# Kernel tuning notes

Hardware: AMD Instinct MI355X
Metric: run time of the kernel (lower is better)

## Reference

```python
import jax, jax.numpy as jnp
import numpy as np

S, B, T, D, NUM_CH = 16, 64, 640, 256, 4
T_WAV = 1.0 / 16000.0
LOG_F_MEAN = 5.02654
LOG_F_STD = 0.373288


def _make_i_2pi(output_dim, num_channels):
    num_freq = output_dim // num_channels
    # harmonic index i+1 repeated num_channels times, times 2*pi -> (D, 1)
    i_vec = np.repeat(np.arange(1, num_freq + 1, dtype=np.float32), num_channels)
    return jnp.asarray(i_vec * (2.0 * np.pi)).reshape(output_dim, 1)


def _make_k_T(time_len):
    # sample times 0..T-1 scaled by 1/16000 -> (1, T)
    return (jnp.arange(time_len, dtype=jnp.float32) * T_WAV).reshape(1, time_len)


def setup_inputs() -> dict:
    key = jax.random.key(0)
    k1, k2, k3, k4, k5 = jax.random.split(key, 5)
    x = jax.random.normal(k1, (S, B, 1, T), dtype=jnp.float32)
    nlf = jax.random.normal(k2, (S, B, 1, 1), dtype=jnp.float32)
    tau = jax.random.uniform(k3, (S, B, 1, 1), dtype=jnp.float32) * (T * T_WAV)
    a = jax.random.normal(k4, (D, 1), dtype=jnp.float32)
    phi = jax.random.normal(k5, (D, 1), dtype=jnp.float32)
    return {"x": x, "nlf": nlf, "tau": tau, "a": a, "phi": phi,
            "i_2pi": _make_i_2pi(D, NUM_CH), "k_T": _make_k_T(T)}


def reference(x, nlf, tau, a, phi, i_2pi, k_T):
    # f: denormalized fundamental frequency, (S,B,1,1)
    f = jnp.exp(nlf * LOG_F_STD + LOG_F_MEAN)
    # t: shifted time axis, (S,B,1,T)
    t = k_T - tau
    # deg = i*2pi*f*t + phi -> (S,B,D,T)
    i_f = i_2pi * f            # (S,B,D,1)
    deg = i_f * t + phi        # (S,B,D,T)
    W = a * jnp.sin(deg)       # (S,B,D,T)
    h_SBDT = W * x             # (S,B,D,T)  <- the huge intermediate
    return jnp.sum(h_SBDT, axis=-1)  # (S,B,D)
```

## Files before the change

kernel.cpp:

```cpp
#include <hip/hip_runtime.h>

constexpr int S_  = 16;
constexpr int B_  = 64;
constexpr int T_  = 640;
constexpr int D_  = 256;
constexpr int H_  = 64;
constexpr int SB_ = S_ * B_;

__device__ __forceinline__ float fractf_(float x) { return __builtin_amdgcn_fractf(x); }
__device__ __forceinline__ float sin2pi_(float r) { return __builtin_amdgcn_sinf(r); }

struct GQ { double g, q; };

__global__ void sinenet_pre(const float* __restrict__ nlf,
                            const float* __restrict__ tau,
                            const float* __restrict__ a,
                            const float* __restrict__ phi,
                            GQ* __restrict__ gq,
                            float* __restrict__ ca,
                            float* __restrict__ sa)
{
    const int idx = blockIdx.x * 256 + threadIdx.x;
    if (idx < SB_) {
        const double fd = exp((double)nlf[idx] * 0.373288 + 5.02654);
        GQ v;
        v.g = fd * (1.0 / 16000.0);
        v.q = fd * (double)tau[idx];
        gq[idx] = v;
    } else if (idx < SB_ + D_) {
        const int d  = idx - SB_;
        const float av = a[d];
        const float pr = phi[d] * 0.15915494309189535f;
        sa[d] = av * sin2pi_(fractf_(pr));
        ca[d] = av * sin2pi_(fractf_(pr + 0.25f));
    }
}

__global__ __launch_bounds__(256, 4)
void sinenet_main(const float* __restrict__ x,
                  const GQ* __restrict__ gq,
                  const float* __restrict__ ca,
                  const float* __restrict__ sa,
                  float* __restrict__ out)
{
    __shared__ __align__(16) float xs[T_];
    __shared__ float redS[4][H_];
    __shared__ float redC[4][H_];

    const int sb   = blockIdx.x;
    const int tid  = threadIdx.x;
    const int w    = tid >> 6;
    const int lane = tid & 63;

    const float4* xg4 = reinterpret_cast<const float4*>(x + (size_t)sb * T_);
    if (tid < T_ / 4) reinterpret_cast<float4*>(xs)[tid] = xg4[tid];

    const double g = gq[sb].g;
    const double q = gq[sb].q;

    const int kA = w * 160;
    const int kB = kA + 80;

    const double hp = (double)(lane + 1);
    double mu = hp * g;  mu -= floor(mu);
    double rA = mu * (double)kA - hp * q;  rA -= floor(rA);
    double rB = rA + mu * 80.0;            rB -= floor(rB);

    const float muf = (float)mu;
    const float sm  = sin2pi_(fractf_(muf));
    const float cm  = sin2pi_(fractf_(muf + 0.25f));
    float sA = sin2pi_(fractf_((float)rA));
    float cA = sin2pi_(fractf_((float)rA + 0.25f));
    float sB = sin2pi_(fractf_((float)rB));
    float cB = sin2pi_(fractf_((float)rB + 0.25f));

    float SsA = 0.0f, CsA = 0.0f, SsB = 0.0f, CsB = 0.0f;

    __syncthreads();

    const float4* xa = reinterpret_cast<const float4*>(xs + kA);
    const float4* xb = reinterpret_cast<const float4*>(xs + kB);

#define STEP(sv, cv, Sacc, Cacc, xval)                                  \
    Sacc = fmaf(sv, xval, Sacc); Cacc = fmaf(cv, xval, Cacc);           \
    { float ns_ = fmaf(sv, cm, cv * sm);                                \
      cv = fmaf(cv, cm, -(sv * sm)); sv = ns_; }

#pragma unroll 4
    for (int i = 0; i < 20; ++i) {
        const float4 va = xa[i];
        const float4 vb = xb[i];
        STEP(sA, cA, SsA, CsA, va.x)  STEP(sB, cB, SsB, CsB, vb.x)
        STEP(sA, cA, SsA, CsA, va.y)  STEP(sB, cB, SsB, CsB, vb.y)
        STEP(sA, cA, SsA, CsA, va.z)  STEP(sB, cB, SsB, CsB, vb.z)
        STEP(sA, cA, SsA, CsA, va.w)  STEP(sB, cB, SsB, CsB, vb.w)
    }
#undef STEP

    redS[w][lane] = SsA + SsB;
    redC[w][lane] = CsA + CsB;
    __syncthreads();

    const int d = tid;
    const int h = tid >> 2;
    const float Sh = redS[0][h] + redS[1][h] + redS[2][h] + redS[3][h];
    const float Ch = redC[0][h] + redC[1][h] + redC[2][h] + redC[3][h];
    out[(size_t)sb * D_ + d] = fmaf(ca[d], Sh, sa[d] * Ch);
}

extern "C" void kernel_launch(void* const* d_in, const int* in_sizes, int n_in,
                              void* d_out, int out_size, void* d_ws, size_t ws_size,
                              hipStream_t stream)
{
    const float* x   = (const float*)d_in[0];
    const float* nlf = (const float*)d_in[1];
    const float* tau = (const float*)d_in[2];
    const float* a   = (const float*)d_in[3];
    const float* phi = (const float*)d_in[4];
    float* out = (float*)d_out;

    GQ*    gq = (GQ*)d_ws;
    float* ca = (float*)((char*)d_ws + SB_ * sizeof(GQ));
    float* sa = ca + D_;

    hipLaunchKernelGGL(sinenet_pre, dim3((SB_ + D_ + 255) / 256), dim3(256), 0, stream,
                       nlf, tau, a, phi, gq, ca, sa);
    hipLaunchKernelGGL(sinenet_main, dim3(SB_), dim3(256), 0, stream,
                       x, gq, ca, sa, out);
}
```

Before: 73.17 us.

## Fuse precompute into main kernel and use Chebyshev sine recurrence

```diff
diff --git a/kernel.cpp b/kernel.cpp
--- a/kernel.cpp
+++ b/kernel.cpp
@@ -10,38 +10,13 @@
 __device__ __forceinline__ float fractf_(float x) { return __builtin_amdgcn_fractf(x); }
 __device__ __forceinline__ float sin2pi_(float r) { return __builtin_amdgcn_sinf(r); }
 
-struct GQ { double g, q; };
-
-__global__ void sinenet_pre(const float* __restrict__ nlf,
-                            const float* __restrict__ tau,
-                            const float* __restrict__ a,
-                            const float* __restrict__ phi,
-                            GQ* __restrict__ gq,
-                            float* __restrict__ ca,
-                            float* __restrict__ sa)
-{
-    const int idx = blockIdx.x * 256 + threadIdx.x;
-    if (idx < SB_) {
-        const double fd = exp((double)nlf[idx] * 0.373288 + 5.02654);
-        GQ v;
-        v.g = fd * (1.0 / 16000.0);
-        v.q = fd * (double)tau[idx];
-        gq[idx] = v;
-    } else if (idx < SB_ + D_) {
-        const int d  = idx - SB_;
-        const float av = a[d];
-        const float pr = phi[d] * 0.15915494309189535f;
-        sa[d] = av * sin2pi_(fractf_(pr));
-        ca[d] = av * sin2pi_(fractf_(pr + 0.25f));
-    }
-}
-
 __global__ __launch_bounds__(256, 4)
-void sinenet_main(const float* __restrict__ x,
-                  const GQ* __restrict__ gq,
-                  const float* __restrict__ ca,
-                  const float* __restrict__ sa,
-                  float* __restrict__ out)
+void sinenet_fused(const float* __restrict__ x,
+                   const float* __restrict__ nlf,
+                   const float* __restrict__ tau,
+                   const float* __restrict__ a,
+                   const float* __restrict__ phi,
+                   float* __restrict__ out)
 {
     __shared__ __align__(16) float xs[T_];
     __shared__ float redS[4][H_];
@@ -55,76 +30,77 @@
     const float4* xg4 = reinterpret_cast<const float4*>(x + (size_t)sb * T_);
     if (tid < T_ / 4) reinterpret_cast<float4*>(xs)[tid] = xg4[tid];
 
-    const double g = gq[sb].g;
-    const double q = gq[sb].q;
+    const float av = a[tid];
+    const float pv = phi[tid];
+
+    const double fd = exp((double)nlf[sb] * 0.373288 + 5.02654);
+    const double g  = fd * (1.0 / 16000.0);
+    const double q  = fd * (double)tau[sb];
 
     const int kA = w * 160;
-    const int kB = kA + 80;
 
     const double hp = (double)(lane + 1);
-    double mu = hp * g;  mu -= floor(mu);
+    double mu = hp * g;                    mu -= floor(mu);
     double rA = mu * (double)kA - hp * q;  rA -= floor(rA);
     double rB = rA + mu * 80.0;            rB -= floor(rB);
 
     const float muf = (float)mu;
     const float sm  = sin2pi_(fractf_(muf));
     const float cm  = sin2pi_(fractf_(muf + 0.25f));
-    float sA = sin2pi_(fractf_((float)rA));
-    float cA = sin2pi_(fractf_((float)rA + 0.25f));
-    float sB = sin2pi_(fractf_((float)rB));
-    float cB = sin2pi_(fractf_((float)rB + 0.25f));
+    const float K   = 2.0f * cm;
+
+    float sA1 = sin2pi_(fractf_((float)rA));
+    float cA1 = sin2pi_(fractf_((float)rA + 0.25f));
+    float sB1 = sin2pi_(fractf_((float)rB));
+    float cB1 = sin2pi_(fractf_((float)rB + 0.25f));
+    float sA0 = fmaf(sA1, cm, -(cA1 * sm));
+    float cA0 = fmaf(cA1, cm,   sA1 * sm);
+    float sB0 = fmaf(sB1, cm, -(cB1 * sm));
+    float cB0 = fmaf(cB1, cm,   sB1 * sm);
 
     float SsA = 0.0f, CsA = 0.0f, SsB = 0.0f, CsB = 0.0f;
 
     __syncthreads();
 
     const float4* xa = reinterpret_cast<const float4*>(xs + kA);
-    const float4* xb = reinterpret_cast<const float4*>(xs + kB);
+    const float4* xb = xa + 20;
 
-#define STEP(sv, cv, Sacc, Cacc, xval)                                  \
-    Sacc = fmaf(sv, xval, Sacc); Cacc = fmaf(cv, xval, Cacc);           \
-    { float ns_ = fmaf(sv, cm, cv * sm);                                \
-      cv = fmaf(cv, cm, -(sv * sm)); sv = ns_; }
+#define STEP2(sp, sc, cp, cc, Sa, Ca, xv)                 \
+    Sa = fmaf(sc, xv, Sa); Ca = fmaf(cc, xv, Ca);         \
+    sp = fmaf(K, sc, -sp); cp = fmaf(K, cc, -cp);
 
 #pragma unroll 4
     for (int i = 0; i < 20; ++i) {
         const float4 va = xa[i];
         const float4 vb = xb[i];
-        STEP(sA, cA, SsA, CsA, va.x)  STEP(sB, cB, SsB, CsB, vb.x)
-        STEP(sA, cA, SsA, CsA, va.y)  STEP(sB, cB, SsB, CsB, vb.y)
-        STEP(sA, cA, SsA, CsA, va.z)  STEP(sB, cB, SsB, CsB, vb.z)
-        STEP(sA, cA, SsA, CsA, va.w)  STEP(sB, cB, SsB, CsB, vb.w)
+        STEP2(sA0, sA1, cA0, cA1, SsA, CsA, va.x)  STEP2(sB0, sB1, cB0, cB1, SsB, CsB, vb.x)
+        STEP2(sA1, sA0, cA1, cA0, SsA, CsA, va.y)  STEP2(sB1, sB0, cB1, cB0, SsB, CsB, vb.y)
+        STEP2(sA0, sA1, cA0, cA1, SsA, CsA, va.z)  STEP2(sB0, sB1, cB0, cB1, SsB, CsB, vb.z)
+        STEP2(sA1, sA0, cA1, cA0, SsA, CsA, va.w)  STEP2(sB1, sB0, cB1, cB0, SsB, CsB, vb.w)
     }
-#undef STEP
+#undef STEP2
 
     redS[w][lane] = SsA + SsB;
     redC[w][lane] = CsA + CsB;
+
+    const float pr  = pv * 0.15915494309189535f;
+    const float sad = av * sin2pi_(fractf_(pr));
+    const float cad = av * sin2pi_(fractf_(pr + 0.25f));
+
     __syncthreads();
 
-    const int d = tid;
     const int h = tid >> 2;
     const float Sh = redS[0][h] + redS[1][h] + redS[2][h] + redS[3][h];
     const float Ch = redC[0][h] + redC[1][h] + redC[2][h] + redC[3][h];
-    out[(size_t)sb * D_ + d] = fmaf(ca[d], Sh, sa[d] * Ch);
+    out[(size_t)sb * D_ + tid] = fmaf(cad, Sh, sad * Ch);
 }
 
 extern "C" void kernel_launch(void* const* d_in, const int* in_sizes, int n_in,
                               void* d_out, int out_size, void* d_ws, size_t ws_size,
                               hipStream_t stream)
 {
-    const float* x   = (const float*)d_in[0];
-    const float* nlf = (const float*)d_in[1];
-    const float* tau = (const float*)d_in[2];
-    const float* a   = (const float*)d_in[3];
-    const float* phi = (const float*)d_in[4];
-    float* out = (float*)d_out;
-
-    GQ*    gq = (GQ*)d_ws;
-    float* ca = (float*)((char*)d_ws + SB_ * sizeof(GQ));
-    float* sa = ca + D_;
-
-    hipLaunchKernelGGL(sinenet_pre, dim3((SB_ + D_ + 255) / 256), dim3(256), 0, stream,
-                       nlf, tau, a, phi, gq, ca, sa);
-    hipLaunchKernelGGL(sinenet_main, dim3(SB_), dim3(256), 0, stream,
-                       x, gq, ca, sa, out);
+    hipLaunchKernelGGL(sinenet_fused, dim3(SB_), dim3(256), 0, stream,
+                       (const float*)d_in[0], (const float*)d_in[1],
+                       (const float*)d_in[2], (const float*)d_in[3],
+                       (const float*)d_in[4], (float*)d_out);
 }
```

Result: faster. 69.46 us (-5.1%).
